# Kernel tuning notes

Hardware: AMD Instinct MI355X
Metric: run time of the kernel (lower is better)

Reference implementation:

```python
import jax, jax.numpy as jnp
import numpy as np

# RRF2d config (matches init_kwargs)
H, W = 64, 64
C_IN, C_OUT = 32, 64
K = 3
PAD = 1  # stride=1, dilation=1 -> S_out == (H, W), L == H*W
L = H * W


def _unfold(x):
    """torch.nn.Unfold(kernel=3, pad=1, stride=1): (B,C,H,W) -> (B, C*K*K, L).
    Channel-major ordering: (c, kh, kw) varies slowest-to-fastest, like torch."""
    xp = jnp.pad(x, ((0, 0), (0, 0), (PAD, PAD), (PAD, PAD)))
    # stack the K*K shifted views: (B, C, K*K, H, W)
    views = [xp[:, :, i:i + H, j:j + W] for i in range(K) for j in range(K)]
    patches = jnp.stack(views, axis=2)
    return patches.reshape(x.shape[0], C_IN * K * K, L)


def setup_inputs() -> dict:
    key = jax.random.key(0)
    k1, k2, k3 = jax.random.split(key, 3)
    x = jax.random.normal(k1, (32, C_IN, H, W), dtype=jnp.float32)
    weights = jax.random.uniform(k2, (C_OUT, C_IN * K * K, L), dtype=jnp.float32)
    biases = jax.random.uniform(k3, (C_OUT, L), dtype=jnp.float32)
    return {"x": x, "weights": weights, "biases": biases}


def reference(x, weights, biases):
    patches = _unfold(x)  # (B, C_in*K*K, L)
    # per-location weighted sum, no weight sharing: contract the patch dim
    y = jnp.einsum("blp,olp->bop", patches, weights) + biases  # (B, C_out, L)
    B = x.shape[0]
    # Fold with kernel (1,1) is just a reshape back to spatial
    return y.reshape(B, C_OUT, H, W)
```

## Files before the change

### kernel.cpp

```cpp
#include <hip/hip_runtime.h>


#define C_IN   32
#define H_SZ   64
#define W_SZ   64
#define C_OUT  64
#define L_SZ   4096
#define KL     288
#define XCH    (H_SZ * W_SZ)

__device__ __forceinline__ void gload_lds4(const float* g, float* l) {
    __builtin_amdgcn_global_load_lds(
        (const __attribute__((address_space(1))) void*)g,
        (__attribute__((address_space(3))) void*)l, 4, 0, 0);
}

__device__ __forceinline__ float dpp_shr1(float v) {
    int i = __builtin_bit_cast(int, v);
    int r = __builtin_amdgcn_update_dpp(i, i, 0x138, 0xF, 0xF, false);
    return __builtin_bit_cast(float, r);
}
__device__ __forceinline__ float dpp_shl1(float v) {
    int i = __builtin_bit_cast(int, v);
    int r = __builtin_amdgcn_update_dpp(i, i, 0x130, 0xF, 0xF, false);
    return __builtin_bit_cast(float, r);
}

__global__ __launch_bounds__(256, 4)
void rrf2d_kernel(const float* __restrict__ x,
                  const float* __restrict__ wgt,
                  const float* __restrict__ bias,
                  float* __restrict__ out) {
    __shared__ float wlds[2][9 * 2 * 128];

    const int t   = threadIdx.x;
    const int wyu = __builtin_amdgcn_readfirstlane(threadIdx.y);
    const int rb  = t >> 5;
    const int k   = t & 31;
    const int c0  = k * 2;
    const int h0  = blockIdx.x * 2;
    const int o0  = blockIdx.y * 2;
    const int b0  = wyu * 8;
    const int h   = h0 + rb;
    const int p   = h * W_SZ + c0;
    const int pl  = rb * 64 + c0;
    const int p0  = h0 * W_SZ;

    int roff[3]; float rvm[3];
    #pragma unroll
    for (int dh = 0; dh < 3; ++dh) {
        const int r = h + dh - 1;
        rvm[dh] = ((unsigned)r < (unsigned)H_SZ) ? 1.f : 0.f;
        const int rc = r < 0 ? 0 : (r > H_SZ - 1 ? H_SZ - 1 : r);
        roff[dh] = rc * W_SZ + c0;
    }
    const bool lval = (k != 0), rval = (k != 31);

    float2 acc[8][2];
    #pragma unroll
    for (int i = 0; i < 8; ++i)
        #pragma unroll
        for (int j = 0; j < 2; ++j) { acc[i][j].x = 0.f; acc[i][j].y = 0.f; }

    const size_t obase[2] = { (size_t)o0 * (KL * (size_t)L_SZ) + p0,
                              (size_t)(o0 + 1) * (KL * (size_t)L_SZ) + p0 };

    auto stage = [&](int cc) {
        float* dst = wlds[cc & 1];
        const size_t coff = (size_t)cc * 9 * L_SZ;
        #pragma unroll
        for (int s = 0; s < 9; ++s) {
            const int r = wyu * 9 + s;
            const int j = r >> 2, o = (r >> 1) & 1, q = r & 1;
            const float* g = wgt + obase[o] + coff + (size_t)j * L_SZ + q * 64 + t;
            gload_lds4(g, dst + (j * 2 + o) * 128 + q * 64);
        }
    };

    stage(0);
    asm volatile("s_waitcnt vmcnt(0)" ::: "memory");
    __builtin_amdgcn_s_barrier();

    for (int c = 0; c < C_IN; ++c) {
        if (c + 1 < C_IN) {
            stage(c + 1);
            asm volatile("s_waitcnt vmcnt(9)" ::: "memory");
        } else {
            asm volatile("s_waitcnt vmcnt(0)" ::: "memory");
        }
        __builtin_amdgcn_s_barrier();

        const float* wb  = wlds[c & 1];
        const float* xco = x + (size_t)c * XCH;

        #pragma unroll
        for (int dh = 0; dh < 3; ++dh) {
            float2 wv[3][2];
            #pragma unroll
            for (int dw = 0; dw < 3; ++dw) {
                const int j = dh * 3 + dw;
                wv[dw][0] = *(const float2*)(wb + (j * 2 + 0) * 128 + pl);
                wv[dw][1] = *(const float2*)(wb + (j * 2 + 1) * 128 + pl);
            }

            float xs[8][4];
            #pragma unroll
            for (int i = 0; i < 8; ++i) {
                const float* xr_ = xco + ((size_t)(b0 + i) * C_IN) * XCH + roff[dh];
                float2 v = *(const float2*)xr_;
                v.x *= rvm[dh];
                v.y *= rvm[dh];
                const float xl = dpp_shr1(v.y);
                const float xr = dpp_shl1(v.x);
                xs[i][0] = lval ? xl : 0.f;
                xs[i][1] = v.x;
                xs[i][2] = v.y;
                xs[i][3] = rval ? xr : 0.f;
            }

            #pragma unroll
            for (int i = 0; i < 8; ++i)
                #pragma unroll
                for (int dw = 0; dw < 3; ++dw) {
                    acc[i][0].x = fmaf(xs[i][dw],     wv[dw][0].x, acc[i][0].x);
                    acc[i][0].y = fmaf(xs[i][dw + 1], wv[dw][0].y, acc[i][0].y);
                    acc[i][1].x = fmaf(xs[i][dw],     wv[dw][1].x, acc[i][1].x);
                    acc[i][1].y = fmaf(xs[i][dw + 1], wv[dw][1].y, acc[i][1].y);
                }
        }
        __builtin_amdgcn_s_barrier();
    }

    #pragma unroll
    for (int j = 0; j < 2; ++j) {
        const float2 bv = *(const float2*)(bias + (size_t)(o0 + j) * L_SZ + p);
        #pragma unroll
        for (int i = 0; i < 8; ++i) {
            float2 r;
            r.x = acc[i][j].x + bv.x;
            r.y = acc[i][j].y + bv.y;
            *(float2*)(out + ((size_t)(b0 + i) * C_OUT + (o0 + j)) * L_SZ + p) = r;
        }
    }
}

extern "C" void kernel_launch(void* const* d_in, const int* in_sizes, int n_in,
                              void* d_out, int out_size, void* d_ws, size_t ws_size,
                              hipStream_t stream) {
    const float* x    = (const float*)d_in[0];
    const float* wgt  = (const float*)d_in[1];
    const float* bias = (const float*)d_in[2];
    float* out        = (float*)d_out;

    dim3 block(64, 4);
    dim3 grid(H_SZ / 2, C_OUT / 2);

    hipLaunchKernelGGL(rrf2d_kernel, grid, block, 0, stream, x, wgt, bias, out);
}
```

Measured before the change: 163.0 us.

## Stage input rows into LDS via async global-to-LDS loads

Result: slower. 166.5 us (median of 2 runs) (+2.2%).

```diff
diff --git a/kernel.cpp b/kernel.cpp
--- a/kernel.cpp
+++ b/kernel.cpp
@@ -26,12 +26,13 @@
     return __builtin_bit_cast(float, r);
 }
 
-__global__ __launch_bounds__(256, 4)
+__global__ __launch_bounds__(256, 3)
 void rrf2d_kernel(const float* __restrict__ x,
                   const float* __restrict__ wgt,
                   const float* __restrict__ bias,
                   float* __restrict__ out) {
     __shared__ float wlds[2][9 * 2 * 128];
+    __shared__ float xlds[32][4][64];
 
     const int t   = threadIdx.x;
     const int wyu = __builtin_amdgcn_readfirstlane(threadIdx.y);
@@ -46,13 +47,18 @@
     const int pl  = rb * 64 + c0;
     const int p0  = h0 * W_SZ;
 
-    int roff[3]; float rvm[3];
+    int rowsrc[4];
+    #pragma unroll
+    for (int s = 0; s < 4; ++s) {
+        int r = h0 - 1 + s;
+        r = r < 0 ? 0 : (r > H_SZ - 1 ? H_SZ - 1 : r);
+        rowsrc[s] = r * W_SZ;
+    }
+    float rvm[3];
     #pragma unroll
     for (int dh = 0; dh < 3; ++dh) {
         const int r = h + dh - 1;
         rvm[dh] = ((unsigned)r < (unsigned)H_SZ) ? 1.f : 0.f;
-        const int rc = r < 0 ? 0 : (r > H_SZ - 1 ? H_SZ - 1 : r);
-        roff[dh] = rc * W_SZ + c0;
     }
     const bool lval = (k != 0), rval = (k != 31);
 
@@ -65,7 +71,7 @@
     const size_t obase[2] = { (size_t)o0 * (KL * (size_t)L_SZ) + p0,
                               (size_t)(o0 + 1) * (KL * (size_t)L_SZ) + p0 };
 
-    auto stage = [&](int cc) {
+    auto stage_w = [&](int cc) {
         float* dst = wlds[cc & 1];
         const size_t coff = (size_t)cc * 9 * L_SZ;
         #pragma unroll
@@ -77,21 +83,32 @@
         }
     };
 
-    stage(0);
+    auto stage_x = [&](int cc) {
+        const float* xc = x + (size_t)cc * XCH;
+        #pragma unroll
+        for (int i = 0; i < 8; ++i) {
+            const float* xb = xc + (size_t)(b0 + i) * (C_IN * XCH);
+            #pragma unroll
+            for (int s = 0; s < 4; ++s)
+                gload_lds4(xb + rowsrc[s] + t, &xlds[b0 + i][s][0]);
+        }
+    };
+
+    stage_w(0);
+    stage_x(0);
     asm volatile("s_waitcnt vmcnt(0)" ::: "memory");
     __builtin_amdgcn_s_barrier();
 
     for (int c = 0; c < C_IN; ++c) {
         if (c + 1 < C_IN) {
-            stage(c + 1);
+            stage_w(c + 1);
             asm volatile("s_waitcnt vmcnt(9)" ::: "memory");
         } else {
             asm volatile("s_waitcnt vmcnt(0)" ::: "memory");
         }
         __builtin_amdgcn_s_barrier();
 
-        const float* wb  = wlds[c & 1];
-        const float* xco = x + (size_t)c * XCH;
+        const float* wb = wlds[c & 1];
 
         #pragma unroll
         for (int dh = 0; dh < 3; ++dh) {
@@ -106,7 +123,7 @@
             float xs[8][4];
             #pragma unroll
             for (int i = 0; i < 8; ++i) {
-                const float* xr_ = xco + ((size_t)(b0 + i) * C_IN) * XCH + roff[dh];
+                const float* xr_ = &xlds[b0 + i][0][0] + (rb + dh) * 64 + c0;
                 float2 v = *(const float2*)xr_;
                 v.x *= rvm[dh];
                 v.y *= rvm[dh];
@@ -116,6 +133,11 @@
                 xs[i][1] = v.x;
                 xs[i][2] = v.y;
                 xs[i][3] = rval ? xr : 0.f;
+            }
+
+            if (dh == 2 && c + 1 < C_IN) {
+                asm volatile("s_waitcnt lgkmcnt(0)" ::: "memory");
+                stage_x(c + 1);
             }
 
             #pragma unroll
```
